# Kernel tuning notes

Hardware: AMD Instinct MI355X
Metric: run time of the kernel (lower is better)

## Reference

```python
import jax, jax.numpy as jnp
import numpy as np


def setup_inputs() -> dict:
    key = jax.random.key(0)
    ks = jax.random.split(key, 24)
    N, C, D_IN, HID, EMB = 8192, 4096, 32, 128, 128
    s = 0.05
    inp = {
        "cand_feat": jax.random.normal(ks[0], (1, C, D_IN), jnp.float32),
        "graph_pos": jax.random.uniform(ks[1], (N, 3), jnp.float32),
        "graph_rad": jax.random.uniform(ks[2], (N,), jnp.float32) + 0.01,
        "L": jnp.ones((1,), jnp.float32),
        "adj": jax.random.uniform(ks[3], (N, N), jnp.float32),
        "mask": jax.random.randint(ks[4], (1, C), 0, 2, jnp.int32),
        # candidate encoder: 32 -> 128 -> 128
        "cW1": jax.random.normal(ks[5], (D_IN, 128), jnp.float32) * s,
        "cb1": jnp.zeros((128,), jnp.float32),
        "cW2": jax.random.normal(ks[6], (128, EMB), jnp.float32) * s,
        "cb2": jnp.zeros((EMB,), jnp.float32),
        # graph encoder input proj: 4 -> 128
        "gW0": jax.random.normal(ks[7], (4, HID), jnp.float32) * s,
        "gb0": jnp.zeros((HID,), jnp.float32),
        # 3 GNN layers: concat(2*HID) -> HID
        "gnnW": jax.random.normal(ks[8], (3, 2 * HID, HID), jnp.float32) * s,
        "gnnb": jnp.zeros((3, HID), jnp.float32),
        # output proj: 2*HID -> EMB
        "goW": jax.random.normal(ks[9], (2 * HID, EMB), jnp.float32) * s,
        "gob": jnp.zeros((EMB,), jnp.float32),
        # fusion: 2*EMB -> 256 -> 128 -> 1
        "fW1": jax.random.normal(ks[10], (2 * EMB, 256), jnp.float32) * s,
        "fb1": jnp.zeros((256,), jnp.float32),
        "fW2": jax.random.normal(ks[11], (256, 128), jnp.float32) * s,
        "fb2": jnp.zeros((128,), jnp.float32),
        "fW3": jax.random.normal(ks[12], (128, 1), jnp.float32) * s,
        "fb3": jnp.zeros((1,), jnp.float32),
    }
    return inp


def reference(cand_feat, graph_pos, graph_rad, L, adj, mask,
              cW1, cb1, cW2, cb2, gW0, gb0, gnnW, gnnb, goW, gob,
              fW1, fb1, fW2, fb2, fW3, fb3):
    relu = jax.nn.relu
    # ---- candidate encoder: [1, C, 32] -> [1, C, 128]
    cand_emb = relu(relu(cand_feat @ cW1 + cb1) @ cW2 + cb2)
    # ---- graph encoder ----
    node = jnp.concatenate([graph_pos / L, (graph_rad / jnp.max(graph_rad))[:, None]], axis=1)  # [N, 4]
    h = relu(node @ gW0 + gb0)  # [N, HID]
    deg = jnp.clip(jnp.sum(adj, axis=-1, keepdims=True), 1.0)  # [N, 1]
    for i in range(gnnW.shape[0]):
        agg = (adj @ h) / deg                       # degree-normalized aggregation
        h = relu(jnp.concatenate([h, agg], axis=-1) @ gnnW[i] + gnnb[i])
    h_glob = jnp.concatenate([jnp.max(h, axis=0), jnp.mean(h, axis=0)], axis=-1)  # [2*HID]
    graph_emb = h_glob @ goW + gob  # [EMB]
    # ---- fusion decoder ----
    g_exp = jnp.broadcast_to(graph_emb[None, None, :], cand_emb.shape)
    combined = jnp.concatenate([cand_emb, g_exp], axis=-1)  # [1, C, 2*EMB]
    scores = (relu(relu(combined @ fW1 + fb1) @ fW2 + fb2) @ fW3 + fb3)[..., 0]  # [1, C]
    return jnp.where(mask == 0, -jnp.inf, scores)
```

## Files before the change

kernel.cpp:

```cpp
#include <hip/hip_runtime.h>
#include <hip/hip_bf16.h>

constexpr int NN  = 8192;
constexpr int CC  = 4096;
constexpr int HD  = 128;
constexpr int KSPLIT = 8;
constexpr int KSTEPS = (NN / KSPLIT) / 64;

typedef __attribute__((ext_vector_type(8))) short bf16x8;
typedef __attribute__((ext_vector_type(4))) short s16x4;
typedef __attribute__((ext_vector_type(4))) float f32x4;

static __device__ __forceinline__ unsigned short f2bf(float f) {
  unsigned int u = __builtin_bit_cast(unsigned int, f);
  unsigned int lsb = (u >> 16) & 1u;
  u += 0x7fffu + lsb;
  return (unsigned short)(u >> 16);
}
static __device__ __forceinline__ float bf2f(unsigned short u) {
  return __builtin_bit_cast(float, ((unsigned int)u) << 16);
}

static __device__ __forceinline__ int swz(int r, int k) {
  return r * 128 + ((((k >> 3) ^ (r & 7))) << 4) + ((k & 7) * 2);
}

#define GL16(gp, lp)                                                              \
  __builtin_amdgcn_global_load_lds(                                               \
      (const __attribute__((address_space(1))) void*)(gp),                        \
      (__attribute__((address_space(3))) void*)(lp), 16, 0, 0)

__global__ __launch_bounds__(256) void k_radmax(const float* __restrict__ rad, float* out) {
  __shared__ float red[256];
  int t = threadIdx.x;
  float m = 0.0f;
  for (int i = t; i < NN; i += 256) m = fmaxf(m, rad[i]);
  red[t] = m; __syncthreads();
  for (int s = 128; s > 0; s >>= 1) {
    if (t < s) red[t] = fmaxf(red[t], red[t + s]);
    __syncthreads();
  }
  if (t == 0) out[0] = red[0];
}

__global__ __launch_bounds__(256) void k_h0(const float* __restrict__ pos, const float* __restrict__ rad,
                                            const float* __restrict__ Lp, const float* __restrict__ rmax,
                                            const float* __restrict__ gW0, const float* __restrict__ gb0,
                                            float* __restrict__ h, unsigned short* __restrict__ hT) {
  __shared__ __align__(16) unsigned short lt[128][72];
  int t = threadIdx.x;
  int i0 = blockIdx.x * 64;
  float invL = 1.0f / Lp[0];
  float invR = 1.0f / rmax[0];
  for (int rep = 0; rep < 32; ++rep) {
    int idx = rep * 256 + t;
    int il = idx >> 7, j = idx & 127;
    int i = i0 + il;
    float n0 = pos[i * 3 + 0] * invL, n1 = pos[i * 3 + 1] * invL, n2 = pos[i * 3 + 2] * invL;
    float n3 = rad[i] * invR;
    float v = gb0[j] + n0 * gW0[j] + n1 * gW0[128 + j] + n2 * gW0[256 + j] + n3 * gW0[384 + j];
    v = fmaxf(v, 0.0f);
    h[(size_t)i * HD + j] = v;
    lt[j][il] = f2bf(v);
  }
  __syncthreads();
  int j = t >> 1, half = t & 1;
  unsigned short* dst = hT + (size_t)j * NN + i0 + half * 32;
  const uint4* src = (const uint4*)&lt[j][half * 32];
  uint4* d4 = (uint4*)dst;
  d4[0] = src[0]; d4[1] = src[1]; d4[2] = src[2]; d4[3] = src[3];
}

template <int CONVERT>
__global__ __launch_bounds__(256) void k_conv(const float* __restrict__ adj,
                                              unsigned short* __restrict__ adjb,
                                              float* __restrict__ deg) {
  int row = blockIdx.x;
  int t = threadIdx.x;
  const float4* src = (const float4*)(adj + (size_t)row * NN);
  float s = 0.f;
  #pragma unroll
  for (int it = 0; it < 4; ++it) {
    int g = (it * 256 + t) * 2;
    float4 v0 = src[g], v1 = src[g + 1];
    s += v0.x + v0.y + v0.z + v0.w + v1.x + v1.y + v1.z + v1.w;
    if (CONVERT) {
      union { unsigned short u[8]; uint4 q; } pk;
      pk.u[0] = f2bf(v0.x); pk.u[1] = f2bf(v0.y); pk.u[2] = f2bf(v0.z); pk.u[3] = f2bf(v0.w);
      pk.u[4] = f2bf(v1.x); pk.u[5] = f2bf(v1.y); pk.u[6] = f2bf(v1.z); pk.u[7] = f2bf(v1.w);
      *(uint4*)(adjb + (size_t)row * NN + (size_t)g * 4) = pk.q;
    }
  }
  for (int o = 32; o > 0; o >>= 1) s += __shfl_down(s, o);
  __shared__ float red[4];
  if ((t & 63) == 0) red[t >> 6] = s;
  __syncthreads();
  if (t == 0) deg[row] = fmaxf(red[0] + red[1] + red[2] + red[3], 1.0f);
}

#define COMPUTE(Ab, Bb)                                                              \
  _Pragma("unroll")                                                                  \
  for (int kk = 0; kk < 2; ++kk) {                                                   \
    int klo = kk * 32 + lk4;                                                         \
    bf16x8 afr[2];                                                                   \
    _Pragma("unroll")                                                                \
    for (int mi = 0; mi < 2; ++mi) {                                                 \
      int r = wr + mi * 16 + lr;                                                     \
      union { bf16x8 v; s16x4 p[2]; } ua;                                            \
      ua.p[0] = *(const s16x4*)((Ab) + swz(r, klo));                                 \
      ua.p[1] = *(const s16x4*)((Ab) + swz(r, klo + 16));                            \
      afr[mi] = ua.v;                                                                \
    }                                                                                \
    _Pragma("unroll")                                                                \
    for (int ni = 0; ni < 4; ++ni) {                                                 \
      int rn = wc + ni * 16 + lr;                                                    \
      union { bf16x8 v; s16x4 p[2]; } ub;                                            \
      ub.p[0] = *(const s16x4*)((Bb) + swz(rn, klo));                                \
      ub.p[1] = *(const s16x4*)((Bb) + swz(rn, klo + 16));                           \
      _Pragma("unroll")                                                              \
      for (int mi = 0; mi < 2; ++mi)                                                 \
        acc[mi][ni] = __builtin_amdgcn_mfma_f32_16x16x32_bf16(afr[mi], ub.v,         \
                                                              acc[mi][ni], 0, 0, 0); \
    }                                                                                \
  }

template <int SRC>
__global__ __launch_bounds__(256) void k_gemm(const float* __restrict__ A32,
                                              const unsigned short* __restrict__ A16,
                                              const unsigned short* __restrict__ hT,
                                              unsigned short* __restrict__ part) {
  __shared__ __align__(16) char As[2][8192];
  __shared__ __align__(16) char Bs[2][16384];
  const int t = threadIdx.x;
  const int bm = blockIdx.x;
  const int ks = blockIdx.y;
  const int kbase = ks * (NN / KSPLIT);

  const int lane = t & 63, w = t >> 6;
  const int wr = (w >> 1) * 32, wc = (w & 1) * 64;
  const int lr = lane & 15, lk4 = (lane >> 4) * 4;

  f32x4 acc[2][4];
  #pragma unroll
  for (int a = 0; a < 2; ++a)
    #pragma unroll
    for (int b = 0; b < 4; ++b) acc[a][b] = f32x4{0.f, 0.f, 0.f, 0.f};

  const int srow = t >> 3;
  const int sgl  = (t & 7) ^ (srow & 7);
  const unsigned short* bSrc[4];
  #pragma unroll
  for (int it = 0; it < 4; ++it)
    bSrc[it] = hT + (size_t)(it * 32 + srow) * NN + kbase + sgl * 8;

  if (SRC == 1) {
    const unsigned short* aSrc[2];
    #pragma unroll
    for (int it = 0; it < 2; ++it)
      aSrc[it] = A16 + (size_t)(bm * 64 + it * 32 + srow) * NN + kbase + sgl * 8;

#define STG(s, d) do {                                  \
    GL16(aSrc[0] + (s) * 64, &As[d][t * 16]);           \
    GL16(aSrc[1] + (s) * 64, &As[d][4096 + t * 16]);    \
    GL16(bSrc[0] + (s) * 64, &Bs[d][t * 16]);           \
    GL16(bSrc[1] + (s) * 64, &Bs[d][4096 + t * 16]);    \
    GL16(bSrc[2] + (s) * 64, &Bs[d][8192 + t * 16]);    \
    GL16(bSrc[3] + (s) * 64, &Bs[d][12288 + t * 16]);   \
  } while (0)

    STG(0, 0);
    int cur = 0;
    for (int step = 0; step < KSTEPS; ++step) {
      if (step + 1 < KSTEPS) {
        STG(step + 1, cur ^ 1);
        asm volatile("s_waitcnt vmcnt(6)" ::: "memory");
      } else {
        asm volatile("s_waitcnt vmcnt(0)" ::: "memory");
      }
      __builtin_amdgcn_s_barrier();
      __builtin_amdgcn_sched_barrier(0);
      COMPUTE(As[cur], Bs[cur]);
      __builtin_amdgcn_sched_barrier(0);
      __builtin_amdgcn_s_barrier();
      cur ^= 1;
    }
#undef STG
  } else {
    const int ar = t >> 2, agq = (t & 3) * 2;
    const float* a32Src = A32 + (size_t)(bm * 64 + ar) * NN + kbase + agq * 8;
    for (int step = 0; step < KSTEPS; ++step) {
      __syncthreads();
      const float* src = a32Src + step * 64;
      float4 v0 = ((const float4*)src)[0], v1 = ((const float4*)src)[1];
      float4 v2 = ((const float4*)src)[2], v3 = ((const float4*)src)[3];
      union { unsigned short u[16]; uint4 q[2]; } pk;
      pk.u[0]  = f2bf(v0.x); pk.u[1]  = f2bf(v0.y); pk.u[2]  = f2bf(v0.z); pk.u[3]  = f2bf(v0.w);
      pk.u[4]  = f2bf(v1.x); pk.u[5]  = f2bf(v1.y); pk.u[6]  = f2bf(v1.z); pk.u[7]  = f2bf(v1.w);
      pk.u[8]  = f2bf(v2.x); pk.u[9]  = f2bf(v2.y); pk.u[10] = f2bf(v2.z); pk.u[11] = f2bf(v2.w);
      pk.u[12] = f2bf(v3.x); pk.u[13] = f2bf(v3.y); pk.u[14] = f2bf(v3.z); pk.u[15] = f2bf(v3.w);
      *(uint4*)(&As[0][ar * 128 + ((agq ^ (ar & 7)) << 4)])       = pk.q[0];
      *(uint4*)(&As[0][ar * 128 + (((agq + 1) ^ (ar & 7)) << 4)]) = pk.q[1];
      #pragma unroll
      for (int it = 0; it < 4; ++it)
        GL16(bSrc[it] + step * 64, &Bs[0][it * 4096 + t * 16]);
      __syncthreads();
      COMPUTE(As[0], Bs[0]);
    }
  }

  unsigned short* outb = part + (size_t)ks * NN * HD;
  #pragma unroll
  for (int mi = 0; mi < 2; ++mi) {
    int rowb = bm * 64 + wr + mi * 16 + (lane >> 4) * 4;
    #pragma unroll
    for (int ni = 0; ni < 4; ++ni) {
      int col = wc + ni * 16 + lr;
      #pragma unroll
      for (int j = 0; j < 4; ++j)
        outb[(size_t)(rowb + j) * HD + col] = f2bf(acc[mi][ni][j]);
    }
  }
}

__global__ __launch_bounds__(256) void k_update(const unsigned short* __restrict__ part,
                                                const float* __restrict__ deg,
                                                const float* __restrict__ hin,
                                                const float* __restrict__ W, const float* __restrict__ bias,
                                                float* __restrict__ hout, unsigned short* __restrict__ hT,
                                                int last) {
  __shared__ float cc[16][256];
  __shared__ __align__(16) unsigned short lt2[128][24];
  int t = threadIdx.x;
  int r0 = blockIdx.x * 16;
  for (int rep = 0; rep < 8; ++rep) {
    int idx = rep * 256 + t;
    int rl = idx >> 7, j = idx & 127;
    int row = r0 + rl;
    float s = 0.f;
    for (int ks = 0; ks < KSPLIT; ++ks)
      s += bf2f(part[((size_t)ks * NN + row) * HD + j]);
    cc[rl][128 + j] = s / deg[row];
    cc[rl][j] = hin[(size_t)row * HD + j];
  }
  __syncthreads();
  int jo = t & 127, rbase = t >> 7;
  float accv[8];
  float bj = bias[jo];
  for (int rr = 0; rr < 8; ++rr) accv[rr] = bj;
  for (int jj = 0; jj < 256; ++jj) {
    float wv = W[jj * HD + jo];
    for (int rr = 0; rr < 8; ++rr) accv[rr] += cc[rbase + rr * 2][jj] * wv;
  }
  for (int rr = 0; rr < 8; ++rr) {
    int rl = rbase + rr * 2;
    float v = fmaxf(accv[rr], 0.f);
    hout[(size_t)(r0 + rl) * HD + jo] = v;
    if (!last) lt2[jo][rl] = f2bf(v);
  }
  if (!last) {
    __syncthreads();
    int j = t >> 1, half = t & 1;
    *(uint4*)(hT + (size_t)j * NN + r0 + half * 8) = *(const uint4*)&lt2[j][half * 8];
  }
}

__global__ __launch_bounds__(256) void k_pool(const float* __restrict__ h,
                                              float* __restrict__ pmax, float* __restrict__ psum) {
  int b = blockIdx.x, t = threadIdx.x;
  int j = t & 127, half = t >> 7;
  int r0 = b * 128 + half * 64;
  float mx = -1e30f, sm = 0.f;
  for (int r = r0; r < r0 + 64; ++r) {
    float v = h[(size_t)r * HD + j];
    mx = fmaxf(mx, v); sm += v;
  }
  __shared__ float lm[2][128], ls[2][128];
  lm[half][j] = mx; ls[half][j] = sm;
  __syncthreads();
  if (half == 0) {
    pmax[b * 128 + j] = fmaxf(lm[0][j], lm[1][j]);
    psum[b * 128 + j] = ls[0][j] + ls[1][j];
  }
}

__global__ __launch_bounds__(256) void k_glob(const float* __restrict__ pmax, const float* __restrict__ psum,
                                              const float* __restrict__ goW, const float* __restrict__ gob,
                                              float* __restrict__ ge) {
  __shared__ float hg[256];
  int t = threadIdx.x;
  int j = t & 127, which = t >> 7;
  if (which == 0) {
    float m = -1e30f;
    for (int b = 0; b < 64; ++b) m = fmaxf(m, pmax[b * 128 + j]);
    hg[j] = m;
  } else {
    float s = 0.f;
    for (int b = 0; b < 64; ++b) s += psum[b * 128 + j];
    hg[128 + j] = s * (1.0f / (float)NN);
  }
  __syncthreads();
  if (t < 128) {
    float s = gob[t];
    for (int jj = 0; jj < 256; ++jj) s += hg[jj] * goW[jj * HD + t];
    ge[t] = s;
  }
}

__global__ __launch_bounds__(256) void k_fusion(const float* __restrict__ cand, const float* __restrict__ ge,
                                                const int* __restrict__ mask,
                                                const float* __restrict__ cW1, const float* __restrict__ cb1,
                                                const float* __restrict__ cW2, const float* __restrict__ cb2,
                                                const float* __restrict__ fW1, const float* __restrict__ fb1,
                                                const float* __restrict__ fW2, const float* __restrict__ fb2,
                                                const float* __restrict__ fW3, const float* __restrict__ fb3,
                                                float* __restrict__ out) {
  __shared__ float x[16][32];
  __shared__ float t1[16][128];
  __shared__ float t2[16][128];
  __shared__ float u1[16][256];
  __shared__ float u2[16][129];
  __shared__ float geL[128];
  int t = threadIdx.x;
  int c0 = blockIdx.x * 16;
  if (t < 128) geL[t] = ge[t];
  for (int rep = 0; rep < 2; ++rep) {
    int idx = rep * 256 + t;
    int cl = idx >> 5, d = idx & 31;
    x[cl][d] = cand[(size_t)(c0 + cl) * 32 + d];
  }
  __syncthreads();
  {
    int j = t & 127, cg = (t >> 7) * 8;
    float a[8]; float bj = cb1[j];
    for (int q = 0; q < 8; ++q) a[q] = bj;
    for (int d = 0; d < 32; ++d) {
      float wv = cW1[d * 128 + j];
      for (int q = 0; q < 8; ++q) a[q] += x[cg + q][d] * wv;
    }
    for (int q = 0; q < 8; ++q) t1[cg + q][j] = fmaxf(a[q], 0.f);
  }
  __syncthreads();
  {
    int j = t & 127, cg = (t >> 7) * 8;
    float a[8]; float bj = cb2[j];
    for (int q = 0; q < 8; ++q) a[q] = bj;
    for (int d = 0; d < 128; ++d) {
      float wv = cW2[d * 128 + j];
      for (int q = 0; q < 8; ++q) a[q] += t1[cg + q][d] * wv;
    }
    for (int q = 0; q < 8; ++q) t2[cg + q][j] = fmaxf(a[q], 0.f);
  }
  __syncthreads();
  {
    int jo = t;
    float gp = fb1[jo];
    for (int d = 0; d < 128; ++d) gp += geL[d] * fW1[(128 + d) * 256 + jo];
    float a[16];
    for (int q = 0; q < 16; ++q) a[q] = gp;
    for (int d = 0; d < 128; ++d) {
      float wv = fW1[d * 256 + jo];
      for (int q = 0; q < 16; ++q) a[q] += t2[q][d] * wv;
    }
    for (int q = 0; q < 16; ++q) u1[q][jo] = fmaxf(a[q], 0.f);
  }
  __syncthreads();
  {
    int j = t & 127, cg = (t >> 7) * 8;
    float a[8]; float bj = fb2[j];
    for (int q = 0; q < 8; ++q) a[q] = bj;
    for (int d = 0; d < 256; ++d) {
      float wv = fW2[d * 128 + j];
      for (int q = 0; q < 8; ++q) a[q] += u1[cg + q][d] * wv;
    }
    for (int q = 0; q < 8; ++q) u2[cg + q][j] = fmaxf(a[q], 0.f);
  }
  __syncthreads();
  if (t < 16) {
    int c = c0 + t;
    float s = fb3[0];
    for (int d = 0; d < 128; ++d) s += u2[t][d] * fW3[d];
    out[c] = (mask[c] == 0) ? -3.0e38f : s;
  }
}

extern "C" void kernel_launch(void* const* d_in, const int* in_sizes, int n_in,
                              void* d_out, int out_size, void* d_ws, size_t ws_size,
                              hipStream_t stream) {
  const float* cand = (const float*)d_in[0];
  const float* pos  = (const float*)d_in[1];
  const float* rad  = (const float*)d_in[2];
  const float* Lp   = (const float*)d_in[3];
  const float* adj  = (const float*)d_in[4];
  const int*   mask = (const int*)d_in[5];
  const float* cW1 = (const float*)d_in[6];
  const float* cb1 = (const float*)d_in[7];
  const float* cW2 = (const float*)d_in[8];
  const float* cb2 = (const float*)d_in[9];
  const float* gW0 = (const float*)d_in[10];
  const float* gb0 = (const float*)d_in[11];
  const float* gnnW = (const float*)d_in[12];
  const float* gnnb = (const float*)d_in[13];
  const float* goW = (const float*)d_in[14];
  const float* gob = (const float*)d_in[15];
  const float* fW1 = (const float*)d_in[16];
  const float* fb1 = (const float*)d_in[17];
  const float* fW2 = (const float*)d_in[18];
  const float* fb2 = (const float*)d_in[19];
  const float* fW3 = (const float*)d_in[20];
  const float* fb3 = (const float*)d_in[21];

  char* ws = (char*)d_ws;
  float* h           = (float*)ws;
  unsigned short* hT = (unsigned short*)(ws + (4ull << 20));
  float* rmax        = (float*)(ws + (6ull << 20));
  float* pmax        = (float*)(ws + (6ull << 20) + 4096);
  float* psum        = pmax + 64 * 128;
  float* ge          = psum + 64 * 128;
  float* deg         = (float*)(ws + (7ull << 20));
  unsigned short* part = (unsigned short*)(ws + (8ull << 20));
  unsigned short* adjb = (unsigned short*)(ws + (24ull << 20));

  bool big = ws_size >= (24ull << 20) + (size_t)NN * NN * 2;

  k_radmax<<<1, 256, 0, stream>>>(rad, rmax);
  k_h0<<<NN / 64, 256, 0, stream>>>(pos, rad, Lp, rmax, gW0, gb0, h, hT);
  if (big) k_conv<1><<<NN, 256, 0, stream>>>(adj, adjb, deg);
  else     k_conv<0><<<NN, 256, 0, stream>>>(adj, nullptr, deg);

  dim3 g(NN / 64, KSPLIT);
  for (int l = 0; l < 3; ++l) {
    if (big) k_gemm<1><<<g, 256, 0, stream>>>(nullptr, adjb, hT, part);
    else     k_gemm<0><<<g, 256, 0, stream>>>(adj, nullptr, hT, part);
    k_update<<<NN / 16, 256, 0, stream>>>(part, deg, h,
                                          gnnW + l * 256 * HD, gnnb + l * HD, h, hT, l == 2);
  }
  k_pool<<<64, 256, 0, stream>>>(h, pmax, psum);
  k_glob<<<1, 256, 0, stream>>>(pmax, psum, goW, gob, ge);
  k_fusion<<<CC / 16, 256, 0, stream>>>(cand, ge, mask, cW1, cb1, cW2, cb2,
                                        fW1, fb1, fW2, fb2, fW3, fb3, (float*)d_out);
}
```

Before: 421.2 us.

## Fuse adjacency bf16 conversion and degree sum into first GEMM; triple-buffer later GEMMs

Removes the separate pass that read the fp32 adjacency to compute degrees and write a bf16 copy. The first-layer GEMM now reads fp32 adj directly, converts it on the fly, writes the bf16 copy and accumulates per-split partial row sums. k_update then reduces those partial degrees itself. Layers 2 and 3 use a new GEMM with a three-stage async load pipeline and wave-uniform LDS destination offsets. The cost is that the first GEMM becomes a synchronous fp32-load GEMM with no load/compute overlap.

```diff
diff --git a/kernel.cpp b/kernel.cpp
--- a/kernel.cpp
+++ b/kernel.cpp
@@ -5,7 +5,8 @@
 constexpr int CC  = 4096;
 constexpr int HD  = 128;
 constexpr int KSPLIT = 8;
-constexpr int KSTEPS = (NN / KSPLIT) / 64;
+constexpr int KCHUNK = NN / KSPLIT;
+constexpr int KSTEPS = KCHUNK / 64;
 
 typedef __attribute__((ext_vector_type(8))) short bf16x8;
 typedef __attribute__((ext_vector_type(4))) short s16x4;
@@ -69,33 +70,6 @@
   const uint4* src = (const uint4*)&lt[j][half * 32];
   uint4* d4 = (uint4*)dst;
   d4[0] = src[0]; d4[1] = src[1]; d4[2] = src[2]; d4[3] = src[3];
-}
-
-template <int CONVERT>
-__global__ __launch_bounds__(256) void k_conv(const float* __restrict__ adj,
-                                              unsigned short* __restrict__ adjb,
-                                              float* __restrict__ deg) {
-  int row = blockIdx.x;
-  int t = threadIdx.x;
-  const float4* src = (const float4*)(adj + (size_t)row * NN);
-  float s = 0.f;
-  #pragma unroll
-  for (int it = 0; it < 4; ++it) {
-    int g = (it * 256 + t) * 2;
-    float4 v0 = src[g], v1 = src[g + 1];
-    s += v0.x + v0.y + v0.z + v0.w + v1.x + v1.y + v1.z + v1.w;
-    if (CONVERT) {
-      union { unsigned short u[8]; uint4 q; } pk;
-      pk.u[0] = f2bf(v0.x); pk.u[1] = f2bf(v0.y); pk.u[2] = f2bf(v0.z); pk.u[3] = f2bf(v0.w);
-      pk.u[4] = f2bf(v1.x); pk.u[5] = f2bf(v1.y); pk.u[6] = f2bf(v1.z); pk.u[7] = f2bf(v1.w);
-      *(uint4*)(adjb + (size_t)row * NN + (size_t)g * 4) = pk.q;
-    }
-  }
-  for (int o = 32; o > 0; o >>= 1) s += __shfl_down(s, o);
-  __shared__ float red[4];
-  if ((t & 63) == 0) red[t >> 6] = s;
-  __syncthreads();
-  if (t == 0) deg[row] = fmaxf(red[0] + red[1] + red[2] + red[3], 1.0f);
 }
 
 #define COMPUTE(Ab, Bb)                                                              \
@@ -124,21 +98,27 @@
     }                                                                                \
   }
 
-template <int SRC>
-__global__ __launch_bounds__(256) void k_gemm(const float* __restrict__ A32,
-                                              const unsigned short* __restrict__ A16,
-                                              const unsigned short* __restrict__ hT,
-                                              unsigned short* __restrict__ part) {
-  __shared__ __align__(16) char As[2][8192];
-  __shared__ __align__(16) char Bs[2][16384];
-  const int t = threadIdx.x;
-  const int bm = blockIdx.x;
-  const int ks = blockIdx.y;
-  const int kbase = ks * (NN / KSPLIT);
-
+__global__ __launch_bounds__(256) void k_gemm23(const unsigned short* __restrict__ A16,
+                                                const unsigned short* __restrict__ hT,
+                                                unsigned short* __restrict__ part) {
+  __shared__ __align__(16) char As[3][8192];
+  __shared__ __align__(16) char Bs[3][16384];
+  const int t = threadIdx.x, bm = blockIdx.x, ks = blockIdx.y;
+  const int kbase = ks * KCHUNK;
   const int lane = t & 63, w = t >> 6;
   const int wr = (w >> 1) * 32, wc = (w & 1) * 64;
   const int lr = lane & 15, lk4 = (lane >> 4) * 4;
+  const unsigned wb = (unsigned)__builtin_amdgcn_readfirstlane(w << 10);
+  const int srow = t >> 3, sgl = (t & 7) ^ (srow & 7);
+
+  const unsigned short* aS[2];
+  const unsigned short* bS[4];
+  #pragma unroll
+  for (int it = 0; it < 2; ++it)
+    aS[it] = A16 + (size_t)(bm * 64 + it * 32 + srow) * NN + kbase + sgl * 8;
+  #pragma unroll
+  for (int it = 0; it < 4; ++it)
+    bS[it] = hT + (size_t)(it * 32 + srow) * NN + kbase + sgl * 8;
 
   f32x4 acc[2][4];
   #pragma unroll
@@ -146,67 +126,34 @@
     #pragma unroll
     for (int b = 0; b < 4; ++b) acc[a][b] = f32x4{0.f, 0.f, 0.f, 0.f};
 
-  const int srow = t >> 3;
-  const int sgl  = (t & 7) ^ (srow & 7);
-  const unsigned short* bSrc[4];
-  #pragma unroll
-  for (int it = 0; it < 4; ++it)
-    bSrc[it] = hT + (size_t)(it * 32 + srow) * NN + kbase + sgl * 8;
-
-  if (SRC == 1) {
-    const unsigned short* aSrc[2];
-    #pragma unroll
-    for (int it = 0; it < 2; ++it)
-      aSrc[it] = A16 + (size_t)(bm * 64 + it * 32 + srow) * NN + kbase + sgl * 8;
-
-#define STG(s, d) do {                                  \
-    GL16(aSrc[0] + (s) * 64, &As[d][t * 16]);           \
-    GL16(aSrc[1] + (s) * 64, &As[d][4096 + t * 16]);    \
-    GL16(bSrc[0] + (s) * 64, &Bs[d][t * 16]);           \
-    GL16(bSrc[1] + (s) * 64, &Bs[d][4096 + t * 16]);    \
-    GL16(bSrc[2] + (s) * 64, &Bs[d][8192 + t * 16]);    \
-    GL16(bSrc[3] + (s) * 64, &Bs[d][12288 + t * 16]);   \
+#define ISSUE23(s, d) do {                                 \
+    GL16(aS[0] + (s) * 64, (char*)As[d] + wb);             \
+    GL16(aS[1] + (s) * 64, (char*)As[d] + 4096 + wb);      \
+    GL16(bS[0] + (s) * 64, (char*)Bs[d] + wb);             \
+    GL16(bS[1] + (s) * 64, (char*)Bs[d] + 4096 + wb);      \
+    GL16(bS[2] + (s) * 64, (char*)Bs[d] + 8192 + wb);      \
+    GL16(bS[3] + (s) * 64, (char*)Bs[d] + 12288 + wb);     \
   } while (0)
 
-    STG(0, 0);
-    int cur = 0;
-    for (int step = 0; step < KSTEPS; ++step) {
-      if (step + 1 < KSTEPS) {
-        STG(step + 1, cur ^ 1);
-        asm volatile("s_waitcnt vmcnt(6)" ::: "memory");
-      } else {
-        asm volatile("s_waitcnt vmcnt(0)" ::: "memory");
-      }
-      __builtin_amdgcn_s_barrier();
-      __builtin_amdgcn_sched_barrier(0);
-      COMPUTE(As[cur], Bs[cur]);
-      __builtin_amdgcn_sched_barrier(0);
-      __builtin_amdgcn_s_barrier();
-      cur ^= 1;
-    }
-#undef STG
-  } else {
-    const int ar = t >> 2, agq = (t & 3) * 2;
-    const float* a32Src = A32 + (size_t)(bm * 64 + ar) * NN + kbase + agq * 8;
-    for (int step = 0; step < KSTEPS; ++step) {
-      __syncthreads();
-      const float* src = a32Src + step * 64;
-      float4 v0 = ((const float4*)src)[0], v1 = ((const float4*)src)[1];
-      float4 v2 = ((const float4*)src)[2], v3 = ((const float4*)src)[3];
-      union { unsigned short u[16]; uint4 q[2]; } pk;
-      pk.u[0]  = f2bf(v0.x); pk.u[1]  = f2bf(v0.y); pk.u[2]  = f2bf(v0.z); pk.u[3]  = f2bf(v0.w);
-      pk.u[4]  = f2bf(v1.x); pk.u[5]  = f2bf(v1.y); pk.u[6]  = f2bf(v1.z); pk.u[7]  = f2bf(v1.w);
-      pk.u[8]  = f2bf(v2.x); pk.u[9]  = f2bf(v2.y); pk.u[10] = f2bf(v2.z); pk.u[11] = f2bf(v2.w);
-      pk.u[12] = f2bf(v3.x); pk.u[13] = f2bf(v3.y); pk.u[14] = f2bf(v3.z); pk.u[15] = f2bf(v3.w);
-      *(uint4*)(&As[0][ar * 128 + ((agq ^ (ar & 7)) << 4)])       = pk.q[0];
-      *(uint4*)(&As[0][ar * 128 + (((agq + 1) ^ (ar & 7)) << 4)]) = pk.q[1];
-      #pragma unroll
-      for (int it = 0; it < 4; ++it)
-        GL16(bSrc[it] + step * 64, &Bs[0][it * 4096 + t * 16]);
-      __syncthreads();
-      COMPUTE(As[0], Bs[0]);
-    }
-  }
+  ISSUE23(0, 0);
+  ISSUE23(1, 1);
+  for (int step = 0; step < KSTEPS; ++step) {
+    const int st = step % 3;
+    if (step + 2 < KSTEPS) {
+      ISSUE23(step + 2, (step + 2) % 3);
+      asm volatile("s_waitcnt vmcnt(12)" ::: "memory");
+    } else if (step + 1 < KSTEPS) {
+      asm volatile("s_waitcnt vmcnt(6)" ::: "memory");
+    } else {
+      asm volatile("s_waitcnt vmcnt(0)" ::: "memory");
+    }
+    __builtin_amdgcn_s_barrier();
+    __builtin_amdgcn_sched_barrier(0);
+    COMPUTE(As[st], Bs[st]);
+    __builtin_amdgcn_sched_barrier(0);
+    __builtin_amdgcn_s_barrier();
+  }
+#undef ISSUE23
 
   unsigned short* outb = part + (size_t)ks * NN * HD;
   #pragma unroll
@@ -222,16 +169,100 @@
   }
 }
 
+template <int WB, int DG>
+__global__ __launch_bounds__(256) void k_gemm1(const float* __restrict__ A32,
+                                               const unsigned short* __restrict__ hT,
+                                               unsigned short* __restrict__ adjb,
+                                               float* __restrict__ part_deg,
+                                               unsigned short* __restrict__ part) {
+  __shared__ __align__(16) char As[8192];
+  __shared__ __align__(16) char Bs[16384];
+  const int t = threadIdx.x, bm = blockIdx.x, ks = blockIdx.y;
+  const int kbase = ks * KCHUNK;
+  const int lane = t & 63, w = t >> 6;
+  const int wr = (w >> 1) * 32, wc = (w & 1) * 64;
+  const int lr = lane & 15, lk4 = (lane >> 4) * 4;
+  const unsigned wb = (unsigned)__builtin_amdgcn_readfirstlane(w << 10);
+  const int srow = t >> 3, sgl = (t & 7) ^ (srow & 7);
+
+  const unsigned short* bS[4];
+  #pragma unroll
+  for (int it = 0; it < 4; ++it)
+    bS[it] = hT + (size_t)(it * 32 + srow) * NN + kbase + sgl * 8;
+
+  const int ar = t >> 2, agq = (t & 3) * 2;
+  const float* a32Src = A32 + (size_t)(bm * 64 + ar) * NN + kbase + agq * 8;
+
+  f32x4 acc[2][4];
+  #pragma unroll
+  for (int a = 0; a < 2; ++a)
+    #pragma unroll
+    for (int b = 0; b < 4; ++b) acc[a][b] = f32x4{0.f, 0.f, 0.f, 0.f};
+
+  float rs = 0.f;
+  for (int step = 0; step < KSTEPS; ++step) {
+    __syncthreads();
+    const float* src = a32Src + step * 64;
+    float4 v0 = ((const float4*)src)[0], v1 = ((const float4*)src)[1];
+    float4 v2 = ((const float4*)src)[2], v3 = ((const float4*)src)[3];
+    union { unsigned short u[16]; uint4 q[2]; } pk;
+    pk.u[0]  = f2bf(v0.x); pk.u[1]  = f2bf(v0.y); pk.u[2]  = f2bf(v0.z); pk.u[3]  = f2bf(v0.w);
+    pk.u[4]  = f2bf(v1.x); pk.u[5]  = f2bf(v1.y); pk.u[6]  = f2bf(v1.z); pk.u[7]  = f2bf(v1.w);
+    pk.u[8]  = f2bf(v2.x); pk.u[9]  = f2bf(v2.y); pk.u[10] = f2bf(v2.z); pk.u[11] = f2bf(v2.w);
+    pk.u[12] = f2bf(v3.x); pk.u[13] = f2bf(v3.y); pk.u[14] = f2bf(v3.z); pk.u[15] = f2bf(v3.w);
+    if (DG) rs += v0.x + v0.y + v0.z + v0.w + v1.x + v1.y + v1.z + v1.w
+                + v2.x + v2.y + v2.z + v2.w + v3.x + v3.y + v3.z + v3.w;
+    if (WB) {
+      uint4* wdst = (uint4*)(adjb + (size_t)(bm * 64 + ar) * NN + kbase + step * 64 + agq * 8);
+      wdst[0] = pk.q[0]; wdst[1] = pk.q[1];
+    }
+    *(uint4*)(As + ar * 128 + ((agq ^ (ar & 7)) << 4))       = pk.q[0];
+    *(uint4*)(As + ar * 128 + (((agq + 1) ^ (ar & 7)) << 4)) = pk.q[1];
+    #pragma unroll
+    for (int it = 0; it < 4; ++it)
+      GL16(bS[it] + step * 64, (char*)Bs + it * 4096 + wb);
+    __syncthreads();
+    COMPUTE(As, Bs);
+  }
+
+  if (DG) {
+    float v = rs;
+    v += __shfl_xor(v, 1);
+    v += __shfl_xor(v, 2);
+    if ((t & 3) == 0) part_deg[(size_t)ks * NN + bm * 64 + ar] = v;
+  }
+
+  unsigned short* outb = part + (size_t)ks * NN * HD;
+  #pragma unroll
+  for (int mi = 0; mi < 2; ++mi) {
+    int rowb = bm * 64 + wr + mi * 16 + (lane >> 4) * 4;
+    #pragma unroll
+    for (int ni = 0; ni < 4; ++ni) {
+      int col = wc + ni * 16 + lr;
+      #pragma unroll
+      for (int j = 0; j < 4; ++j)
+        outb[(size_t)(rowb + j) * HD + col] = f2bf(acc[mi][ni][j]);
+    }
+  }
+}
+
 __global__ __launch_bounds__(256) void k_update(const unsigned short* __restrict__ part,
-                                                const float* __restrict__ deg,
+                                                const float* __restrict__ part_deg,
                                                 const float* __restrict__ hin,
                                                 const float* __restrict__ W, const float* __restrict__ bias,
                                                 float* __restrict__ hout, unsigned short* __restrict__ hT,
                                                 int last) {
   __shared__ float cc[16][256];
+  __shared__ float degS[16];
   __shared__ __align__(16) unsigned short lt2[128][24];
   int t = threadIdx.x;
   int r0 = blockIdx.x * 16;
+  if (t < 16) {
+    float d = 0.f;
+    for (int ks = 0; ks < KSPLIT; ++ks) d += part_deg[(size_t)ks * NN + r0 + t];
+    degS[t] = fmaxf(d, 1.0f);
+  }
+  __syncthreads();
   for (int rep = 0; rep < 8; ++rep) {
     int idx = rep * 256 + t;
     int rl = idx >> 7, j = idx & 127;
@@ -239,7 +270,7 @@
     float s = 0.f;
     for (int ks = 0; ks < KSPLIT; ++ks)
       s += bf2f(part[((size_t)ks * NN + row) * HD + j]);
-    cc[rl][128 + j] = s / deg[row];
+    cc[rl][128 + j] = s / degS[rl];
     cc[rl][j] = hin[(size_t)row * HD + j];
   }
   __syncthreads();
@@ -416,7 +447,7 @@
   float* pmax        = (float*)(ws + (6ull << 20) + 4096);
   float* psum        = pmax + 64 * 128;
   float* ge          = psum + 64 * 128;
-  float* deg         = (float*)(ws + (7ull << 20));
+  float* part_deg    = (float*)(ws + (7ull << 20));
   unsigned short* part = (unsigned short*)(ws + (8ull << 20));
   unsigned short* adjb = (unsigned short*)(ws + (24ull << 20));
 
@@ -424,14 +455,17 @@
 
   k_radmax<<<1, 256, 0, stream>>>(rad, rmax);
   k_h0<<<NN / 64, 256, 0, stream>>>(pos, rad, Lp, rmax, gW0, gb0, h, hT);
-  if (big) k_conv<1><<<NN, 256, 0, stream>>>(adj, adjb, deg);
-  else     k_conv<0><<<NN, 256, 0, stream>>>(adj, nullptr, deg);
 
   dim3 g(NN / 64, KSPLIT);
   for (int l = 0; l < 3; ++l) {
-    if (big) k_gemm<1><<<g, 256, 0, stream>>>(nullptr, adjb, hT, part);
-    else     k_gemm<0><<<g, 256, 0, stream>>>(adj, nullptr, hT, part);
-    k_update<<<NN / 16, 256, 0, stream>>>(part, deg, h,
+    if (l == 0) {
+      if (big) k_gemm1<1, 1><<<g, 256, 0, stream>>>(adj, hT, adjb, part_deg, part);
+      else     k_gemm1<0, 1><<<g, 256, 0, stream>>>(adj, hT, nullptr, part_deg, part);
+    } else {
+      if (big) k_gemm23<<<g, 256, 0, stream>>>(adjb, hT, part);
+      else     k_gemm1<0, 0><<<g, 256, 0, stream>>>(adj, hT, nullptr, nullptr, part);
+    }
+    k_update<<<NN / 16, 256, 0, stream>>>(part, part_deg, h,
                                           gnnW + l * 256 * HD, gnnb + l * HD, h, hT, l == 2);
   }
   k_pool<<<64, 256, 0, stream>>>(h, pmax, psum);
```

New measurement: 420.2 us. About the same (-0.2%).
